# Kernel tuning notes

Hardware: AMD Instinct MI355X
Metric: run time of the kernel (lower is better)

## Reference

```python
import jax, jax.numpy as jnp
import numpy as np

MULTI_INFER_NUM = 8
D_EMBED = 128
T, B = 512, 32


def setup_inputs() -> dict:
    key = jax.random.key(0)
    k1, k2, k3 = jax.random.split(key, 3)
    positions = jax.random.randint(k1, (T, B), 0, 16, dtype=jnp.int64)
    outputs = jax.random.normal(k2, (T, B, D_EMBED), dtype=jnp.float32)
    table = jax.random.normal(k3, (MULTI_INFER_NUM + 1, D_EMBED, D_EMBED), dtype=jnp.float32)
    return {"positions": positions, "outputs": outputs, "table": table}


def reference(positions, outputs, table):
    # clip positions >= multi_infer_num to the sentinel row multi_infer_num
    r_positions = jnp.where(positions < MULTI_INFER_NUM, positions, MULTI_INFER_NUM)
    # gather per-(t,b) d x d transfer matrices: [T, B, d, d]
    positions_embedding = table[r_positions]
    # batched matvec: [T, B, d]
    transferred = jnp.einsum('ibde,ibd->ibe', positions_embedding, outputs)
    return transferred
```

## Files before the change

kernel.cpp:

```cpp
#include <hip/hip_runtime.h>
#include <hip/hip_bf16.h>

#define TBPAIRS 16384
#define DEMB    128
#define NR      9
#define CAP     16384
#define CHUNK   64
#define NCHUNK  (TBPAIRS / CHUNK)
#define NVIRT   (NR * NCHUNK)
#define GRID2   512

#define BPACK_U4    (NR * 2048)
#define BPACK_BYTES (BPACK_U4 * 16)

using short8 = __attribute__((ext_vector_type(8))) short;
using f32x4  = __attribute__((ext_vector_type(4))) float;

__device__ __forceinline__ unsigned short f2bf(float f) {
    unsigned u = __float_as_uint(f);
    u = u + 0x7FFFu + ((u >> 16) & 1u);
    return (unsigned short)(u >> 16);
}

__global__ __launch_bounds__(256) void prep_kernel(
    const int*   __restrict__ positions,
    const float* __restrict__ table,
    uint4* __restrict__ bpack,
    int*   __restrict__ gcnt,
    int*   __restrict__ perm) {

    const int bid = blockIdx.x;
    const int tid = threadIdx.x;

    if (bid < 64) {
        __shared__ int lcnt[NR];
        __shared__ int lbase[NR];
        if (tid < NR) lcnt[tid] = 0;
        __syncthreads();
        const int pair = bid * 256 + tid;
        const int p = positions[pair];
        const int r = (p < 8) ? p : 8;
        const int rank = atomicAdd(&lcnt[r], 1);
        __syncthreads();
        if (tid < NR) lbase[tid] = atomicAdd(&gcnt[tid], lcnt[tid]);
        __syncthreads();
        perm[r * CAP + lbase[r] + rank] = pair;
    } else {
        const int pid = bid - 64;
        const int r   = pid >> 2;
        const int seg = pid & 3;
        const float* M = table + r * DEMB * DEMB;
#pragma unroll
        for (int k = 0; k < 2; ++k) {
            const int idx  = seg * 512 + k * 256 + tid;
            const int lane = idx & 63;
            const int ks   = (idx >> 6) & 3;
            const int nt   = idx >> 8;
            const int e    = nt * 16 + (lane & 15);
            const int d0   = ks * 32 + (lane >> 4) * 8;
            union { unsigned short us[8]; uint4 v; } u;
#pragma unroll
            for (int j = 0; j < 8; ++j)
                u.us[j] = f2bf(M[(d0 + j) * DEMB + e]);
            bpack[r * 2048 + idx] = u.v;
        }
    }
}

__global__ __launch_bounds__(256) void transfer_kernel(
    const float* __restrict__ x,
    const uint4* __restrict__ bpack,
    const int*   __restrict__ gcnt,
    const int*   __restrict__ perm,
    float*       __restrict__ out) {

    const int tid  = threadIdx.x;
    const int wave = tid >> 6;
    const int lane = tid & 63;
    const int m16  = lane & 15;
    const int quad = lane >> 4;

    for (int v = blockIdx.x; v < NVIRT; v += GRID2) {
        const int r     = v % NR;
        const int chunk = v / NR;
        const int c     = gcnt[r];
        const int base  = chunk * CHUNK;
        if (base >= c) continue;
        const int tb = base + wave * 16;
        if (tb >= c) continue;
        const int nm = c - tb;

        const int* pr = perm + r * CAP + tb;

        const int slotA = pr[(m16 < nm) ? m16 : 0];
        const float* xrow = x + (size_t)slotA * DEMB;
        short8 a[4];
#pragma unroll
        for (int ks = 0; ks < 4; ++ks) {
            const float4* s4 = (const float4*)(xrow + ks * 32 + quad * 8);
            float4 f0 = s4[0];
            float4 f1 = s4[1];
            union { unsigned short us[8]; short8 s8; } ua;
            ua.us[0] = f2bf(f0.x); ua.us[1] = f2bf(f0.y);
            ua.us[2] = f2bf(f0.z); ua.us[3] = f2bf(f0.w);
            ua.us[4] = f2bf(f1.x); ua.us[5] = f2bf(f1.y);
            ua.us[6] = f2bf(f1.z); ua.us[7] = f2bf(f1.w);
            a[ks] = ua.s8;
        }

        int  prow[4];
        bool pval[4];
#pragma unroll
        for (int i = 0; i < 4; ++i) {
            const int m = quad * 4 + i;
            pval[i] = m < nm;
            prow[i] = pval[i] ? pr[m] : 0;
        }

        const uint4* bp = bpack + r * 2048 + lane;
#pragma unroll 2
        for (int nt = 0; nt < 8; ++nt) {
            f32x4 acc = {0.f, 0.f, 0.f, 0.f};
#pragma unroll
            for (int ks = 0; ks < 4; ++ks) {
                union { uint4 v4; short8 s8; } ub;
                ub.v4 = bp[(nt * 4 + ks) * 64];
                acc = __builtin_amdgcn_mfma_f32_16x16x32_bf16(a[ks], ub.s8, acc, 0, 0, 0);
            }
            const int col = nt * 16 + m16;
#pragma unroll
            for (int i = 0; i < 4; ++i)
                if (pval[i]) out[(size_t)prow[i] * DEMB + col] = acc[i];
        }
    }
}

extern "C" void kernel_launch(void* const* d_in, const int* in_sizes, int n_in,
                              void* d_out, int out_size, void* d_ws, size_t ws_size,
                              hipStream_t stream) {
    const int*   positions = (const int*)d_in[0];
    const float* outputs   = (const float*)d_in[1];
    const float* table     = (const float*)d_in[2];
    float* out = (float*)d_out;

    uint4* bpack = (uint4*)d_ws;
    int*   gcnt  = (int*)((char*)d_ws + BPACK_BYTES);
    int*   perm  = (int*)((char*)d_ws + BPACK_BYTES + 64);

    hipMemsetAsync((void*)gcnt, 0, 64, stream);

    hipLaunchKernelGGL(prep_kernel, dim3(100), dim3(256), 0, stream,
                       positions, table, bpack, gcnt, perm);
    hipLaunchKernelGGL(transfer_kernel, dim3(GRID2), dim3(256), 0, stream,
                       outputs, bpack, gcnt, perm, out);
}
```

Baseline: 80.74 us.

## Replace global atomic bucketing with per-block histograms and in-kernel prefix scan

Prep no longer uses global atomics or a memset. Each block writes its bucket counts and a local permutation, and the transfer kernel builds a prefix sum in shared memory, then finds each row's source by binary search. Each wave now handles two 16-row tiles that share the same B fragment loads, with the chunk size doubled. This removes the memset launch and global atomic contention, and cuts B reloads per row. The cost is a redundant scan in every block and six-step searches per row index.

Result: slower. 93.20 us (+15.4%).

```diff
diff --git a/kernel.cpp b/kernel.cpp
--- a/kernel.cpp
+++ b/kernel.cpp
@@ -4,14 +4,16 @@
 #define TBPAIRS 16384
 #define DEMB    128
 #define NR      9
-#define CAP     16384
-#define CHUNK   64
+#define NBLK    64
+#define CHUNK   128
 #define NCHUNK  (TBPAIRS / CHUNK)
 #define NVIRT   (NR * NCHUNK)
 #define GRID2   512
 
 #define BPACK_U4    (NR * 2048)
 #define BPACK_BYTES (BPACK_U4 * 16)
+#define HIST_OFF    BPACK_BYTES
+#define LPERM_OFF   (HIST_OFF + 4096)
 
 using short8 = __attribute__((ext_vector_type(8))) short;
 using f32x4  = __attribute__((ext_vector_type(4))) float;
@@ -26,27 +28,25 @@
     const int*   __restrict__ positions,
     const float* __restrict__ table,
     uint4* __restrict__ bpack,
-    int*   __restrict__ gcnt,
-    int*   __restrict__ perm) {
+    int*   __restrict__ hist,
+    int*   __restrict__ lperm) {
 
     const int bid = blockIdx.x;
     const int tid = threadIdx.x;
 
-    if (bid < 64) {
-        __shared__ int lcnt[NR];
-        __shared__ int lbase[NR];
-        if (tid < NR) lcnt[tid] = 0;
+    if (bid < NBLK) {
+        __shared__ int cnt[NR];
+        if (tid < NR) cnt[tid] = 0;
         __syncthreads();
         const int pair = bid * 256 + tid;
         const int p = positions[pair];
         const int r = (p < 8) ? p : 8;
-        const int rank = atomicAdd(&lcnt[r], 1);
+        const int rank = atomicAdd(&cnt[r], 1);
+        lperm[(r * NBLK + bid) * 256 + rank] = pair;
         __syncthreads();
-        if (tid < NR) lbase[tid] = atomicAdd(&gcnt[tid], lcnt[tid]);
-        __syncthreads();
-        perm[r * CAP + lbase[r] + rank] = pair;
+        if (tid < NR) hist[bid * NR + tid] = cnt[tid];
     } else {
-        const int pid = bid - 64;
+        const int pid = bid - NBLK;
         const int r   = pid >> 2;
         const int seg = pid & 3;
         const float* M = table + r * DEMB * DEMB;
@@ -70,11 +70,27 @@
 __global__ __launch_bounds__(256) void transfer_kernel(
     const float* __restrict__ x,
     const uint4* __restrict__ bpack,
-    const int*   __restrict__ gcnt,
-    const int*   __restrict__ perm,
+    const int*   __restrict__ hist,
+    const int*   __restrict__ lperm,
     float*       __restrict__ out) {
 
-    const int tid  = threadIdx.x;
+    __shared__ int lhist[NBLK * NR];
+    __shared__ int ps[NR * 65];
+
+    const int tid = threadIdx.x;
+
+    for (int i = tid; i < NBLK * NR; i += 256) lhist[i] = hist[i];
+    __syncthreads();
+    if (tid < NR) {
+        int acc = 0;
+        for (int b = 0; b < NBLK; ++b) {
+            ps[tid * 65 + b] = acc;
+            acc += lhist[b * NR + tid];
+        }
+        ps[tid * 65 + 64] = acc;
+    }
+    __syncthreads();
+
     const int wave = tid >> 6;
     const int lane = tid & 63;
     const int m16  = lane & 15;
@@ -83,54 +99,78 @@
     for (int v = blockIdx.x; v < NVIRT; v += GRID2) {
         const int r     = v % NR;
         const int chunk = v / NR;
-        const int c     = gcnt[r];
+        const int c     = ps[r * 65 + 64];
         const int base  = chunk * CHUNK;
         if (base >= c) continue;
-        const int tb = base + wave * 16;
-        if (tb >= c) continue;
-        const int nm = c - tb;
+        const int tb0 = base + wave * 32;
+        if (tb0 >= c) continue;
 
-        const int* pr = perm + r * CAP + tb;
+        auto mapg = [&](int g) -> int {
+            int lo = 0, hi = 64;
+#pragma unroll
+            for (int s = 0; s < 6; ++s) {
+                const int mid = (lo + hi) >> 1;
+                if (ps[r * 65 + mid] <= g) lo = mid; else hi = mid;
+            }
+            return lperm[(r * NBLK + lo) * 256 + (g - ps[r * 65 + lo])];
+        };
 
-        const int slotA = pr[(m16 < nm) ? m16 : 0];
-        const float* xrow = x + (size_t)slotA * DEMB;
-        short8 a[4];
+        short8 a[2][4];
+        int    prow[2][4];
+        bool   pval[2][4];
+        int    nmv[2];
 #pragma unroll
-        for (int ks = 0; ks < 4; ++ks) {
-            const float4* s4 = (const float4*)(xrow + ks * 32 + quad * 8);
-            float4 f0 = s4[0];
-            float4 f1 = s4[1];
-            union { unsigned short us[8]; short8 s8; } ua;
-            ua.us[0] = f2bf(f0.x); ua.us[1] = f2bf(f0.y);
-            ua.us[2] = f2bf(f0.z); ua.us[3] = f2bf(f0.w);
-            ua.us[4] = f2bf(f1.x); ua.us[5] = f2bf(f1.y);
-            ua.us[6] = f2bf(f1.z); ua.us[7] = f2bf(f1.w);
-            a[ks] = ua.s8;
+        for (int s2 = 0; s2 < 2; ++s2) {
+            const int tb = tb0 + 16 * s2;
+            const int nm = c - tb;
+            nmv[s2] = nm;
+            if (nm > 0) {
+                const int slotA = mapg(tb + ((m16 < nm) ? m16 : 0));
+                const float* xrow = x + (size_t)slotA * DEMB;
+#pragma unroll
+                for (int ks = 0; ks < 4; ++ks) {
+                    const float4* s4 = (const float4*)(xrow + ks * 32 + quad * 8);
+                    const float4 f0 = s4[0];
+                    const float4 f1 = s4[1];
+                    union { unsigned short us[8]; short8 s8; } ua;
+                    ua.us[0] = f2bf(f0.x); ua.us[1] = f2bf(f0.y);
+                    ua.us[2] = f2bf(f0.z); ua.us[3] = f2bf(f0.w);
+                    ua.us[4] = f2bf(f1.x); ua.us[5] = f2bf(f1.y);
+                    ua.us[6] = f2bf(f1.z); ua.us[7] = f2bf(f1.w);
+                    a[s2][ks] = ua.s8;
+                }
+            }
+#pragma unroll
+            for (int i = 0; i < 4; ++i) {
+                const int m = quad * 4 + i;
+                pval[s2][i] = (nm > 0) && (m < nm);
+                prow[s2][i] = pval[s2][i] ? mapg(tb + m) : 0;
+            }
         }
 
-        int  prow[4];
-        bool pval[4];
-#pragma unroll
-        for (int i = 0; i < 4; ++i) {
-            const int m = quad * 4 + i;
-            pval[i] = m < nm;
-            prow[i] = pval[i] ? pr[m] : 0;
-        }
-
-        const uint4* bp = bpack + r * 2048 + lane;
+        const uint4* bp  = bpack + r * 2048 + lane;
+        const bool   two = nmv[1] > 0;
 #pragma unroll 2
         for (int nt = 0; nt < 8; ++nt) {
-            f32x4 acc = {0.f, 0.f, 0.f, 0.f};
+            f32x4 acc0 = {0.f, 0.f, 0.f, 0.f};
+            f32x4 acc1 = {0.f, 0.f, 0.f, 0.f};
 #pragma unroll
             for (int ks = 0; ks < 4; ++ks) {
                 union { uint4 v4; short8 s8; } ub;
                 ub.v4 = bp[(nt * 4 + ks) * 64];
-                acc = __builtin_amdgcn_mfma_f32_16x16x32_bf16(a[ks], ub.s8, acc, 0, 0, 0);
+                acc0 = __builtin_amdgcn_mfma_f32_16x16x32_bf16(a[0][ks], ub.s8, acc0, 0, 0, 0);
+                if (two)
+                    acc1 = __builtin_amdgcn_mfma_f32_16x16x32_bf16(a[1][ks], ub.s8, acc1, 0, 0, 0);
             }
             const int col = nt * 16 + m16;
 #pragma unroll
             for (int i = 0; i < 4; ++i)
-                if (pval[i]) out[(size_t)prow[i] * DEMB + col] = acc[i];
+                if (pval[0][i]) out[(size_t)prow[0][i] * DEMB + col] = acc0[i];
+            if (two) {
+#pragma unroll
+                for (int i = 0; i < 4; ++i)
+                    if (pval[1][i]) out[(size_t)prow[1][i] * DEMB + col] = acc1[i];
+            }
         }
     }
 }
@@ -144,13 +184,11 @@
     float* out = (float*)d_out;
 
     uint4* bpack = (uint4*)d_ws;
-    int*   gcnt  = (int*)((char*)d_ws + BPACK_BYTES);
-    int*   perm  = (int*)((char*)d_ws + BPACK_BYTES + 64);
-
-    hipMemsetAsync((void*)gcnt, 0, 64, stream);
+    int*   hist  = (int*)((char*)d_ws + HIST_OFF);
+    int*   lperm = (int*)((char*)d_ws + LPERM_OFF);
 
     hipLaunchKernelGGL(prep_kernel, dim3(100), dim3(256), 0, stream,
-                       positions, table, bpack, gcnt, perm);
+                       positions, table, bpack, hist, lperm);
     hipLaunchKernelGGL(transfer_kernel, dim3(GRID2), dim3(256), 0, stream,
-                       outputs, bpack, gcnt, perm, out);
+                       outputs, bpack, hist, lperm, out);
 }
```

## Compact work list via prefix-sum of per-row tile counts; nontemporal output stores

Applied to the files above, without the earlier changes.

Rather than iterating over a fixed 9x256 virtual chunk grid where most chunks are empty, each block computes a prefix sum of 16-row tile counts per table row in shared memory. Waves then stride over only the tiles that exist. This removes idle iterations and load imbalance across the grid. Output stores are also switched to nontemporal hints to avoid polluting cache.

Result: faster. 75.53 us (-6.4%).

```diff
diff --git a/kernel.cpp b/kernel.cpp
--- a/kernel.cpp
+++ b/kernel.cpp
@@ -5,9 +5,6 @@
 #define DEMB    128
 #define NR      9
 #define CAP     16384
-#define CHUNK   64
-#define NCHUNK  (TBPAIRS / CHUNK)
-#define NVIRT   (NR * NCHUNK)
 #define GRID2   512
 
 #define BPACK_U4    (NR * 2048)
@@ -74,22 +71,33 @@
     const int*   __restrict__ perm,
     float*       __restrict__ out) {
 
-    const int tid  = threadIdx.x;
-    const int wave = tid >> 6;
-    const int lane = tid & 63;
-    const int m16  = lane & 15;
-    const int quad = lane >> 4;
+    __shared__ int cs[NR];
+    __shared__ int tp[NR + 1];
 
-    for (int v = blockIdx.x; v < NVIRT; v += GRID2) {
-        const int r     = v % NR;
-        const int chunk = v / NR;
-        const int c     = gcnt[r];
-        const int base  = chunk * CHUNK;
-        if (base >= c) continue;
-        const int tb = base + wave * 16;
-        if (tb >= c) continue;
+    const int tid = threadIdx.x;
+    if (tid < NR) cs[tid] = gcnt[tid];
+    __syncthreads();
+    if (tid == 0) {
+        int acc = 0;
+#pragma unroll
+        for (int r = 0; r < NR; ++r) { tp[r] = acc; acc += (cs[r] + 15) >> 4; }
+        tp[NR] = acc;
+    }
+    __syncthreads();
+
+    const int wave  = tid >> 6;
+    const int lane  = tid & 63;
+    const int m16   = lane & 15;
+    const int quad  = lane >> 4;
+    const int total = tp[NR];
+
+    for (int T = blockIdx.x * 4 + wave; T < total; T += GRID2 * 4) {
+        int r = 0;
+#pragma unroll
+        for (int rr = 1; rr < NR; ++rr) r = (T >= tp[rr]) ? rr : r;
+        const int tb = (T - tp[r]) * 16;
+        const int c  = cs[r];
         const int nm = c - tb;
-
         const int* pr = perm + r * CAP + tb;
 
         const int slotA = pr[(m16 < nm) ? m16 : 0];
@@ -98,8 +106,8 @@
 #pragma unroll
         for (int ks = 0; ks < 4; ++ks) {
             const float4* s4 = (const float4*)(xrow + ks * 32 + quad * 8);
-            float4 f0 = s4[0];
-            float4 f1 = s4[1];
+            const float4 f0 = s4[0];
+            const float4 f1 = s4[1];
             union { unsigned short us[8]; short8 s8; } ua;
             ua.us[0] = f2bf(f0.x); ua.us[1] = f2bf(f0.y);
             ua.us[2] = f2bf(f0.z); ua.us[3] = f2bf(f0.w);
@@ -130,7 +138,8 @@
             const int col = nt * 16 + m16;
 #pragma unroll
             for (int i = 0; i < 4; ++i)
-                if (pval[i]) out[(size_t)prow[i] * DEMB + col] = acc[i];
+                if (pval[i])
+                    __builtin_nontemporal_store(acc[i], &out[(size_t)prow[i] * DEMB + col]);
         }
     }
 }
@@ -148,7 +157,6 @@
     int*   perm  = (int*)((char*)d_ws + BPACK_BYTES + 64);
 
     hipMemsetAsync((void*)gcnt, 0, 64, stream);
-
     hipLaunchKernelGGL(prep_kernel, dim3(100), dim3(256), 0, stream,
                        positions, table, bpack, gcnt, perm);
     hipLaunchKernelGGL(transfer_kernel, dim3(GRID2), dim3(256), 0, stream,
```
